# Kernel tuning notes

Hardware: AMD Instinct MI355X
Metric: run time of the kernel (lower is better)

The kernel has to match this reference:

```python
import jax, jax.numpy as jnp
import numpy as np

DT = 0.02
TMAX = 3.0
NUM_T = 151  # arange(0, Tmax+dt, dt) -> indices 0..150, 150*dt == Tmax == nonspike
THRESH = 1.0
TIMELINE = jnp.arange(NUM_T, dtype=jnp.float32) * DT          # [T]
TIMELINE_REV = jnp.flip(TIMELINE) + 0.1                        # [T]


def linear_spike_fwd(ti, W):
    """ti: [B, Fin] spike times; W: [Fout, Fin] -> out: [B, Fout] spike times."""
    # ramp: relu(t - ti)  -> [B, Fin, T]
    tmp = jax.nn.relu(TIMELINE[None, None, :] - ti[:, :, None])
    # membrane voltage: mem[b,j,t] = sum_i W[j,i] * tmp[b,i,t]  -> [B, Fout, T]
    mem = jnp.einsum('bit,ji->bjt', tmp, W)
    binary = (mem >= THRESH).astype(jnp.float32)
    binary = binary.at[:, :, -1].set(1.0)  # force spike at last timestep
    # reversed-timeline weighting makes argmax pick the FIRST spike index
    idx = jnp.argmax(binary * TIMELINE_REV, axis=2)
    return idx.astype(jnp.float32) * DT


def setup_inputs() -> dict:
    key = jax.random.key(0)
    k1, k2, k3 = jax.random.split(key, 3)
    B, F0, F1, F2 = 64, 1876, 1024, 10
    ti = jax.random.uniform(k1, (B, F0), dtype=jnp.float32)  # spike times in [0,1)
    W1 = 0.002 + 0.002 * jax.random.normal(k2, (F1, F0), dtype=jnp.float32)
    W2 = 0.001 + 0.001 * jax.random.normal(k3, (F2, F1), dtype=jnp.float32)
    return {"ti": ti, "W1": W1, "W2": W2}


def reference(ti, W1, W2):
    h1 = linear_spike_fwd(ti, W1)
    h2 = linear_spike_fwd(h1, W2)
    return h2
```

## Files before the change

### kernel.cpp

```cpp
#include <hip/hip_runtime.h>
#include <stdint.h>

namespace {

constexpr int   B_   = 64;
constexpr int   F0_  = 1876;
constexpr int   F0P_ = 1880;
constexpr int   NI4_ = 469;
constexpr int   F1_  = 1024;
constexpr int   F2_  = 10;
constexpr int   NT_  = 151;
constexpr float DT_  = 0.02f;
constexpr float SCL_  = 1073741824.0f;
constexpr float ISCL_ = 1.0f / 1073741824.0f;

constexpr int NBLK_T = 480;
constexpr int NBLK_R = 470;

constexpr size_t OFF_W1I4 = 0;
constexpr size_t OFF_KOFF = 7684096;
constexpr size_t OFF_TV   = 7924736;
constexpr size_t OFF_IDX1 = 8406016;

__global__ __launch_bounds__(256) void k_prep(const float* __restrict__ W1,
                                              const float* __restrict__ ti,
                                              int4* __restrict__ W1iT4,
                                              uint16_t* __restrict__ koff16,
                                              float* __restrict__ tvarr) {
  const int t = threadIdx.x;
  if (blockIdx.x < NBLK_T) {
    __shared__ float tile[64][65];
    const int bx = blockIdx.x;
    const int i0 = (bx % 30) * 64;
    const int j0 = (bx / 30) * 64;
    const int c = t & 63, r4 = t >> 6;
    for (int jj = r4; jj < 64; jj += 4) {
      int i = i0 + c;
      tile[c][jj] = (i < F0_) ? W1[(size_t)(j0 + jj) * F0_ + i] : 0.0f;
    }
    __syncthreads();
    for (int ii4 = r4; ii4 < 16; ii4 += 4) {
      int i4 = (i0 >> 2) + ii4;
      if (i4 < NI4_) {
        int4 v;
        v.x = __float2int_rn(tile[ii4 * 4 + 0][c] * SCL_);
        v.y = __float2int_rn(tile[ii4 * 4 + 1][c] * SCL_);
        v.z = __float2int_rn(tile[ii4 * 4 + 2][c] * SCL_);
        v.w = __float2int_rn(tile[ii4 * 4 + 3][c] * SCL_);
        W1iT4[(size_t)i4 * F1_ + j0 + c] = v;
      }
    }
  } else {
    int n = (blockIdx.x - NBLK_T) * 256 + t;
    int b = n / F0P_, i = n - b * F0P_;
    if (i < F0_) {
      float v = ti[(size_t)b * F0_ + i];
      int k = (int)fminf(ceilf(v * 50.0f), 50.0f);
      koff16[n] = (uint16_t)(k << 8);
      tvarr[n]  = v;
    } else {
      koff16[n] = 0;
      tvarr[n]  = 0.0f;
    }
  }
}

__global__ __launch_bounds__(512, 8) void k_main1(const uint16_t* __restrict__ koff16,
                                                  const float* __restrict__ tvarr,
                                                  const int4* __restrict__ W1iT4,
                                                  uint8_t* __restrict__ idx1) {
  __shared__ int bins[2][51][64];
  const int blk  = blockIdx.x;
  const int b    = blk >> 4;
  const int jg   = blk & 15;
  const int tid  = threadIdx.x;
  const int lane = tid & 63;
  const int wv   = __builtin_amdgcn_readfirstlane(tid >> 6);

  {
    int4* p = (int4*)(&bins[0][0][0]);
    for (int s = tid; s < (2 * 51 * 64) / 4; s += 512)
      p[s] = make_int4(0, 0, 0, 0);
  }
  __syncthreads();

  const int cnt = 58 + (wv < 5 ? 1 : 0);
  const int g0  = wv * 58 + (wv < 5 ? wv : 5);

  const int4*     __restrict__ wp = W1iT4 + (jg << 6) + lane;
  const uint16_t* __restrict__ kb = koff16 + (size_t)b * F0P_;
  const float*    __restrict__ tb = tvarr  + (size_t)b * F0P_;
  char* const binlane = (char*)(&bins[0][0][0]) + (lane << 2);

#define ELEM(a_, tv_, ko_) {                                                  \
    int c_ = __float2int_rn((float)(a_) * (tv_));                             \
    int* cell = (int*)(binlane + (ko_));                                      \
    atomicAdd(cell, (a_));                              \
    atomicAdd(cell + 51 * 64, c_);           }

#pragma unroll 2
  for (int m = 0; m < cnt; ++m) {
    const int i4 = g0 + m;
    int4   wa  = wp[(size_t)i4 << 10];
    uint2  kk  = *(const uint2*)(kb + i4 * 4);
    float4 tv4 = *(const float4*)(tb + i4 * 4);
    ELEM(wa.x, tv4.x, kk.x & 0xFFFFu);
    ELEM(wa.y, tv4.y, kk.x >> 16);
    ELEM(wa.z, tv4.z, kk.y & 0xFFFFu);
    ELEM(wa.w, tv4.w, kk.y >> 16);
  }
#undef ELEM
  __syncthreads();

  if (tid < 64) {
    float sa = 0.f, sc = 0.f;
    int cnd = NT_;
#pragma unroll 1
    for (int tt = 0; tt < NT_; ++tt) {
      if (tt < 51) {
        sa += (float)bins[0][tt][tid] * ISCL_;
        sc += (float)bins[1][tt][tid] * ISCL_;
      }
      float mv = (float)tt * DT_ * sa - sc;
      if (cnd == NT_ && mv >= 1.0f) cnd = tt;
    }
    cnd = min(cnd, NT_ - 1);
    idx1[((size_t)b << 10) + (jg << 6) + tid] = (uint8_t)cnd;
  }
}

__global__ __launch_bounds__(256) void k_main2(const uint8_t* __restrict__ idx1,
                                               const float* __restrict__ W2,
                                               float* __restrict__ out) {
  __shared__ float wrow[F1_];
  __shared__ float tirow[F1_];
  __shared__ float part[4][3][64];
  const int blk = blockIdx.x;
  const int b   = blk / 10;
  const int j   = blk - b * 10;
  const int tid = threadIdx.x;
  const int lane = tid & 63, wvv = tid >> 6;

  const float*   w = W2  + (size_t)j * F1_;
  const uint8_t* h = idx1 + (size_t)b * F1_;
  for (int s = tid; s < F1_; s += 256) {
    wrow[s]  = w[s];
    tirow[s] = (float)h[s] * DT_;
  }
  __syncthreads();

  const float tl0 = (float)lane * DT_;
  const float tl1 = (float)(lane + 64) * DT_;
  const float tl2 = (float)(lane + 128) * DT_;
  float m0 = 0.f, m1 = 0.f, m2 = 0.f;
  const int i0 = wvv * 256;
#pragma unroll 4
  for (int i = i0; i < i0 + 256; ++i) {
    float tiv = tirow[i], ww = wrow[i];
    m0 = fmaf(ww, fmaxf(tl0 - tiv, 0.f), m0);
    m1 = fmaf(ww, fmaxf(tl1 - tiv, 0.f), m1);
    m2 = fmaf(ww, fmaxf(tl2 - tiv, 0.f), m2);
  }
  part[wvv][0][lane] = m0;
  part[wvv][1][lane] = m1;
  part[wvv][2][lane] = m2;
  __syncthreads();

  if (wvv == 0) {
    m0 = part[0][0][lane] + part[1][0][lane] + part[2][0][lane] + part[3][0][lane];
    m1 = part[0][1][lane] + part[1][1][lane] + part[2][1][lane] + part[3][1][lane];
    m2 = part[0][2][lane] + part[1][2][lane] + part[2][2][lane] + part[3][2][lane];
    unsigned long long b0 = __ballot(m0 >= 1.0f);
    unsigned long long b1 = __ballot(m1 >= 1.0f);
    unsigned long long b2 = __ballot(m2 >= 1.0f);
    b2 &= (1ull << 23) - 1;
    b2 |= (1ull << 22);
    int tres;
    if (b0)      tres = __ffsll((long long)b0) - 1;
    else if (b1) tres = 64 + __ffsll((long long)b1) - 1;
    else         tres = 128 + __ffsll((long long)b2) - 1;
    if (lane == 0) out[(size_t)b * F2_ + j] = (float)tres * DT_;
  }
}

}

extern "C" void kernel_launch(void* const* d_in, const int* in_sizes, int n_in,
                              void* d_out, int out_size, void* d_ws, size_t ws_size,
                              hipStream_t stream) {
  const float* ti = (const float*)d_in[0];
  const float* W1 = (const float*)d_in[1];
  const float* W2 = (const float*)d_in[2];
  float* out = (float*)d_out;

  char* ws = (char*)d_ws;
  int4*     W1iT4 = (int4*)(ws + OFF_W1I4);
  uint16_t* koff  = (uint16_t*)(ws + OFF_KOFF);
  float*    tvs   = (float*)(ws + OFF_TV);
  uint8_t*  idx1  = (uint8_t*)(ws + OFF_IDX1);

  hipLaunchKernelGGL(k_prep,  dim3(NBLK_T + NBLK_R), dim3(256), 0, stream,
                     W1, ti, W1iT4, koff, tvs);
  hipLaunchKernelGGL(k_main1, dim3(1024), dim3(512), 0, stream,
                     koff, tvs, W1iT4, idx1);
  hipLaunchKernelGGL(k_main2, dim3(640),  dim3(256), 0, stream, idx1, W2, out);
}
```

Baseline: 69.29 us.

## Compute spike bin offsets inline and read W2/idx1 directly from global

Removes the padded koff/tvarr precompute from the prep kernel. The main kernel now reads raw ti and computes the time-bin index per element itself, which cuts prep work and two intermediate buffers. The second-layer kernel drops its shared-memory staging of W2 and idx1 and reads them as vectorised global loads. The trade is extra ALU work in the hot atomic loop, plus float4 loads from ti rows of stride 1876, which stay 16-byte aligned because 1876 is divisible by 4.

```diff
diff --git a/kernel.cpp b/kernel.cpp
--- a/kernel.cpp
+++ b/kernel.cpp
@@ -5,7 +5,6 @@
 
 constexpr int   B_   = 64;
 constexpr int   F0_  = 1876;
-constexpr int   F0P_ = 1880;
 constexpr int   NI4_ = 469;
 constexpr int   F1_  = 1024;
 constexpr int   F2_  = 10;
@@ -14,59 +13,36 @@
 constexpr float SCL_  = 1073741824.0f;
 constexpr float ISCL_ = 1.0f / 1073741824.0f;
 
-constexpr int NBLK_T = 480;
-constexpr int NBLK_R = 470;
-
 constexpr size_t OFF_W1I4 = 0;
-constexpr size_t OFF_KOFF = 7684096;
-constexpr size_t OFF_TV   = 7924736;
-constexpr size_t OFF_IDX1 = 8406016;
+constexpr size_t OFF_IDX1 = 7684096;
 
 __global__ __launch_bounds__(256) void k_prep(const float* __restrict__ W1,
-                                              const float* __restrict__ ti,
-                                              int4* __restrict__ W1iT4,
-                                              uint16_t* __restrict__ koff16,
-                                              float* __restrict__ tvarr) {
-  const int t = threadIdx.x;
-  if (blockIdx.x < NBLK_T) {
-    __shared__ float tile[64][65];
-    const int bx = blockIdx.x;
-    const int i0 = (bx % 30) * 64;
-    const int j0 = (bx / 30) * 64;
-    const int c = t & 63, r4 = t >> 6;
-    for (int jj = r4; jj < 64; jj += 4) {
-      int i = i0 + c;
-      tile[c][jj] = (i < F0_) ? W1[(size_t)(j0 + jj) * F0_ + i] : 0.0f;
-    }
-    __syncthreads();
-    for (int ii4 = r4; ii4 < 16; ii4 += 4) {
-      int i4 = (i0 >> 2) + ii4;
-      if (i4 < NI4_) {
-        int4 v;
-        v.x = __float2int_rn(tile[ii4 * 4 + 0][c] * SCL_);
-        v.y = __float2int_rn(tile[ii4 * 4 + 1][c] * SCL_);
-        v.z = __float2int_rn(tile[ii4 * 4 + 2][c] * SCL_);
-        v.w = __float2int_rn(tile[ii4 * 4 + 3][c] * SCL_);
-        W1iT4[(size_t)i4 * F1_ + j0 + c] = v;
-      }
-    }
-  } else {
-    int n = (blockIdx.x - NBLK_T) * 256 + t;
-    int b = n / F0P_, i = n - b * F0P_;
-    if (i < F0_) {
-      float v = ti[(size_t)b * F0_ + i];
-      int k = (int)fminf(ceilf(v * 50.0f), 50.0f);
-      koff16[n] = (uint16_t)(k << 8);
-      tvarr[n]  = v;
-    } else {
-      koff16[n] = 0;
-      tvarr[n]  = 0.0f;
+                                              int4* __restrict__ W1iT4) {
+  __shared__ float tile[64][65];
+  const int t  = threadIdx.x;
+  const int bx = blockIdx.x;
+  const int i0 = (bx % 30) * 64;
+  const int j0 = (bx / 30) * 64;
+  const int c = t & 63, r4 = t >> 6;
+  for (int jj = r4; jj < 64; jj += 4) {
+    int i = i0 + c;
+    tile[c][jj] = (i < F0_) ? W1[(size_t)(j0 + jj) * F0_ + i] : 0.0f;
+  }
+  __syncthreads();
+  for (int ii4 = r4; ii4 < 16; ii4 += 4) {
+    int i4 = (i0 >> 2) + ii4;
+    if (i4 < NI4_) {
+      int4 v;
+      v.x = __float2int_rn(tile[ii4 * 4 + 0][c] * SCL_);
+      v.y = __float2int_rn(tile[ii4 * 4 + 1][c] * SCL_);
+      v.z = __float2int_rn(tile[ii4 * 4 + 2][c] * SCL_);
+      v.w = __float2int_rn(tile[ii4 * 4 + 3][c] * SCL_);
+      W1iT4[(size_t)i4 * F1_ + j0 + c] = v;
     }
   }
 }
 
-__global__ __launch_bounds__(512, 8) void k_main1(const uint16_t* __restrict__ koff16,
-                                                  const float* __restrict__ tvarr,
+__global__ __launch_bounds__(512, 8) void k_main1(const float* __restrict__ ti,
                                                   const int4* __restrict__ W1iT4,
                                                   uint8_t* __restrict__ idx1) {
   __shared__ int bins[2][51][64];
@@ -87,14 +63,14 @@
   const int cnt = 58 + (wv < 5 ? 1 : 0);
   const int g0  = wv * 58 + (wv < 5 ? wv : 5);
 
-  const int4*     __restrict__ wp = W1iT4 + (jg << 6) + lane;
-  const uint16_t* __restrict__ kb = koff16 + (size_t)b * F0P_;
-  const float*    __restrict__ tb = tvarr  + (size_t)b * F0P_;
+  const int4*  __restrict__ wp = W1iT4 + (jg << 6) + lane;
+  const float* __restrict__ tb = ti + (size_t)b * F0_;
   char* const binlane = (char*)(&bins[0][0][0]) + (lane << 2);
 
-#define ELEM(a_, tv_, ko_) {                                                  \
+#define ELEM(a_, tv_) {                                                       \
+    int k_ = (int)fminf(ceilf((tv_) * 50.0f), 50.0f);            \
     int c_ = __float2int_rn((float)(a_) * (tv_));                             \
-    int* cell = (int*)(binlane + (ko_));                                      \
+    int* cell = (int*)(binlane + (k_ << 8));                                  \
     atomicAdd(cell, (a_));                              \
     atomicAdd(cell + 51 * 64, c_);           }
 
@@ -102,12 +78,11 @@
   for (int m = 0; m < cnt; ++m) {
     const int i4 = g0 + m;
     int4   wa  = wp[(size_t)i4 << 10];
-    uint2  kk  = *(const uint2*)(kb + i4 * 4);
     float4 tv4 = *(const float4*)(tb + i4 * 4);
-    ELEM(wa.x, tv4.x, kk.x & 0xFFFFu);
-    ELEM(wa.y, tv4.y, kk.x >> 16);
-    ELEM(wa.z, tv4.z, kk.y & 0xFFFFu);
-    ELEM(wa.w, tv4.w, kk.y >> 16);
+    ELEM(wa.x, tv4.x);
+    ELEM(wa.y, tv4.y);
+    ELEM(wa.z, tv4.z);
+    ELEM(wa.w, tv4.w);
   }
 #undef ELEM
   __syncthreads();
@@ -132,8 +107,6 @@
 __global__ __launch_bounds__(256) void k_main2(const uint8_t* __restrict__ idx1,
                                                const float* __restrict__ W2,
                                                float* __restrict__ out) {
-  __shared__ float wrow[F1_];
-  __shared__ float tirow[F1_];
   __shared__ float part[4][3][64];
   const int blk = blockIdx.x;
   const int b   = blk / 10;
@@ -141,25 +114,25 @@
   const int tid = threadIdx.x;
   const int lane = tid & 63, wvv = tid >> 6;
 
-  const float*   w = W2  + (size_t)j * F1_;
-  const uint8_t* h = idx1 + (size_t)b * F1_;
-  for (int s = tid; s < F1_; s += 256) {
-    wrow[s]  = w[s];
-    tirow[s] = (float)h[s] * DT_;
-  }
-  __syncthreads();
+  const float4*   __restrict__ w4 = (const float4*)(W2 + (size_t)j * F1_);
+  const uint32_t* __restrict__ h4 = (const uint32_t*)(idx1 + ((size_t)b << 10));
 
   const float tl0 = (float)lane * DT_;
   const float tl1 = (float)(lane + 64) * DT_;
   const float tl2 = (float)(lane + 128) * DT_;
   float m0 = 0.f, m1 = 0.f, m2 = 0.f;
-  const int i0 = wvv * 256;
+  const int q0 = wvv * 64;
 #pragma unroll 4
-  for (int i = i0; i < i0 + 256; ++i) {
-    float tiv = tirow[i], ww = wrow[i];
-    m0 = fmaf(ww, fmaxf(tl0 - tiv, 0.f), m0);
-    m1 = fmaf(ww, fmaxf(tl1 - tiv, 0.f), m1);
-    m2 = fmaf(ww, fmaxf(tl2 - tiv, 0.f), m2);
+  for (int q = q0; q < q0 + 64; ++q) {
+    float4   w  = w4[q];
+    uint32_t hh = h4[q];
+#define E2(we_, sh_) {                                                        \
+      float tiv = (float)((hh >> (sh_)) & 255u) * DT_;                        \
+      m0 = fmaf((we_), fmaxf(tl0 - tiv, 0.f), m0);                            \
+      m1 = fmaf((we_), fmaxf(tl1 - tiv, 0.f), m1);                            \
+      m2 = fmaf((we_), fmaxf(tl2 - tiv, 0.f), m2); }
+    E2(w.x, 0); E2(w.y, 8); E2(w.z, 16); E2(w.w, 24);
+#undef E2
   }
   part[wvv][0][lane] = m0;
   part[wvv][1][lane] = m1;
@@ -194,14 +167,10 @@
   float* out = (float*)d_out;
 
   char* ws = (char*)d_ws;
-  int4*     W1iT4 = (int4*)(ws + OFF_W1I4);
-  uint16_t* koff  = (uint16_t*)(ws + OFF_KOFF);
-  float*    tvs   = (float*)(ws + OFF_TV);
-  uint8_t*  idx1  = (uint8_t*)(ws + OFF_IDX1);
+  int4*    W1iT4 = (int4*)(ws + OFF_W1I4);
+  uint8_t* idx1  = (uint8_t*)(ws + OFF_IDX1);
 
-  hipLaunchKernelGGL(k_prep,  dim3(NBLK_T + NBLK_R), dim3(256), 0, stream,
-                     W1, ti, W1iT4, koff, tvs);
-  hipLaunchKernelGGL(k_main1, dim3(1024), dim3(512), 0, stream,
-                     koff, tvs, W1iT4, idx1);
+  hipLaunchKernelGGL(k_prep,  dim3(480),  dim3(256), 0, stream, W1, W1iT4);
+  hipLaunchKernelGGL(k_main1, dim3(1024), dim3(512), 0, stream, ti, W1iT4, idx1);
   hipLaunchKernelGGL(k_main2, dim3(640),  dim3(256), 0, stream, idx1, W2, out);
 }
```

New measurement: 69.18 us. About the same (-0.2%).
